# Kernel tuning notes

Hardware: AMD Instinct MI355X
Metric: run time of the kernel (lower is better)

Reference implementation:

```python
import jax, jax.numpy as jnp
import numpy as np

G, N, D, H, R, O = 16384, 32, 128, 256, 32, 64  # graphs, nodes/graph, input_dim, hidden_dim, rank_dim, output_dim


def _xavier_uniform(key, shape):
    fan_in, fan_out = shape[0], shape[1]
    a = jnp.sqrt(6.0 / (fan_in + fan_out))
    return jax.random.uniform(key, shape, minval=-a, maxval=a, dtype=jnp.float32)


def setup_inputs() -> dict:
    key = jax.random.key(0)
    k_h, k_W, k_V, k_Wl, k_bl = jax.random.split(key, 5)
    h = jax.random.normal(k_h, (G, N, D), dtype=jnp.float32)
    W = _xavier_uniform(k_W, (D, R))          # graph_cp_pooling.W
    V = _xavier_uniform(k_V, (H, R))          # graph_cp_pooling.V
    Wl = _xavier_uniform(k_Wl, (O, H))        # linears_prediction[0].weight
    bl = jnp.zeros((O,), dtype=jnp.float32)   # linears_prediction[0].bias
    return {"h": h, "W": W, "V": V, "Wl": Wl, "bl": bl}


def reference(h, W, V, Wl, bl):
    # graph_cp_pooling (init=True), vectorized over graphs:
    #   feat_g = h_g @ W          -> [G, N, R]
    #   pooled = prod over nodes  -> [G, R]
    #   readout = pooled @ V.T    -> [G, H]
    feat = jnp.einsum('gnd,dr->gnr', h, W)
    pooled = jnp.prod(feat, axis=1)
    readout = pooled @ V.T
    # linears_prediction[0]; dropout is identity in eval mode
    score = readout @ Wl.T + bl
    return score
```

## Files before the change

### kernel.cpp

```cpp
#include <hip/hip_runtime.h>
#include <math.h>

#define NG  16384
#define NN  32
#define DD  128
#define RR  32
#define OO  64
#define HHH 256

__global__ void precompute_M_kernel(const float* __restrict__ Wl,
                                    const float* __restrict__ V,
                                    float* __restrict__ M) {
    int t = blockIdx.x * blockDim.x + threadIdx.x;
    int o = t >> 5;
    int r = t & 31;
    float s = 0.f;
#pragma unroll 8
    for (int hh = 0; hh < HHH; ++hh)
        s = fmaf(Wl[o * HHH + hh], V[hh * RR + r], s);
    M[o * RR + r] = s;
}

__device__ __forceinline__ void fma4(float4& a, float s, const float4& w) {
    a.x = fmaf(s, w.x, a.x);
    a.y = fmaf(s, w.y, a.y);
    a.z = fmaf(s, w.z, a.z);
    a.w = fmaf(s, w.w, a.w);
}

typedef const float __attribute__((address_space(1))) gfloat;
typedef float       __attribute__((address_space(3))) lfloat;

__global__ __launch_bounds__(256, 2)
void gin_main_kernel(const float* __restrict__ hsrc,
                     const float* __restrict__ W,
                     const float* __restrict__ M,
                     const float* __restrict__ bl,
                     float* __restrict__ out) {
    __shared__ float sW[DD * RR];
    __shared__ float sH[4][NN * 32];

    const int tid  = threadIdx.x;
    const int lane = tid & 63;
    const int wv   = tid >> 6;

    {
        const float4* Wv  = (const float4*)W;
        float4*       sWv = (float4*)sW;
#pragma unroll
        for (int k = 0; k < 4; ++k) sWv[tid + k * 256] = Wv[tid + k * 256];
    }
    __syncthreads();

    const int rg = lane & 7;
    const int ng = lane >> 3;
    const int r0 = rg * 4;
    float* sHw = sH[wv];
    const int rowl = lane >> 3;
    const int tq   = lane & 7;
    const float* pWb = sW + r0;

    const int wave_global = blockIdx.x * 4 + wv;
    const float blv = bl[lane];

#pragma unroll 1
    for (int gi = 0; gi < 4; ++gi) {
        const int g = wave_global * 4 + gi;
        const float* hg = hsrc + (size_t)g * (NN * DD);

        float4 acc0 = make_float4(0.f, 0.f, 0.f, 0.f);
        float4 acc1 = acc0, acc2 = acc0, acc3 = acc0;

#pragma unroll
        for (int c = 0; c < 4; ++c) {
#pragma unroll
            for (int l = 0; l < 4; ++l) {
                const int row = l * 8 + rowl;
                const int sq  = (tq + row) & 7;
                const float* gp = hg + row * DD + c * 32 + sq * 4;
                __builtin_amdgcn_global_load_lds((gfloat*)gp,
                                                 (lfloat*)(sHw + l * 256),
                                                 16, 0, 0);
            }
            asm volatile("s_waitcnt vmcnt(0)" ::: "memory");

            const float* ph = sHw + ng * 32;
#pragma unroll
            for (int q = 0; q < 8; ++q) {
                const int d = c * 32 + q * 4;
                const int hq = ((q - ng) & 7) * 4;
                float4 w0 = *(const float4*)(pWb + (d + 0) * RR);
                float4 w1 = *(const float4*)(pWb + (d + 1) * RR);
                float4 w2 = *(const float4*)(pWb + (d + 2) * RR);
                float4 w3 = *(const float4*)(pWb + (d + 3) * RR);
                float4 h0 = *(const float4*)(ph + 0 * 256 + hq);
                float4 h1 = *(const float4*)(ph + 1 * 256 + hq);
                float4 h2 = *(const float4*)(ph + 2 * 256 + hq);
                float4 h3 = *(const float4*)(ph + 3 * 256 + hq);
                fma4(acc0, h0.x, w0); fma4(acc0, h0.y, w1); fma4(acc0, h0.z, w2); fma4(acc0, h0.w, w3);
                fma4(acc1, h1.x, w0); fma4(acc1, h1.y, w1); fma4(acc1, h1.z, w2); fma4(acc1, h1.w, w3);
                fma4(acc2, h2.x, w0); fma4(acc2, h2.y, w1); fma4(acc2, h2.z, w2); fma4(acc2, h2.w, w3);
                fma4(acc3, h3.x, w0); fma4(acc3, h3.y, w1); fma4(acc3, h3.z, w2); fma4(acc3, h3.w, w3);
            }
        }

        float4 p;
        p.x = acc0.x * acc1.x * acc2.x * acc3.x;
        p.y = acc0.y * acc1.y * acc2.y * acc3.y;
        p.z = acc0.z * acc1.z * acc2.z * acc3.z;
        p.w = acc0.w * acc1.w * acc2.w * acc3.w;
#pragma unroll
        for (int m = 8; m <= 32; m <<= 1) {
            p.x *= __shfl_xor(p.x, m);
            p.y *= __shfl_xor(p.y, m);
            p.z *= __shfl_xor(p.z, m);
            p.w *= __shfl_xor(p.w, m);
        }

        const float4* Mv = (const float4*)(M + lane * RR);
        float s = blv;
#pragma unroll
        for (int rq = 0; rq < 8; ++rq) {
            float4 pq;
            pq.x = __shfl(p.x, rq);
            pq.y = __shfl(p.y, rq);
            pq.z = __shfl(p.z, rq);
            pq.w = __shfl(p.w, rq);
            float4 m4 = Mv[rq];
            s = fmaf(pq.x, m4.x, s);
            s = fmaf(pq.y, m4.y, s);
            s = fmaf(pq.z, m4.z, s);
            s = fmaf(pq.w, m4.w, s);
        }
        out[(size_t)g * OO + lane] = s;
    }
}

extern "C" void kernel_launch(void* const* d_in, const int* in_sizes, int n_in,
                              void* d_out, int out_size, void* d_ws, size_t ws_size,
                              hipStream_t stream) {
    const float* h  = (const float*)d_in[0];
    const float* W  = (const float*)d_in[1];
    const float* V  = (const float*)d_in[2];
    const float* Wl = (const float*)d_in[3];
    const float* bl = (const float*)d_in[4];
    float* out = (float*)d_out;
    float* M   = (float*)d_ws;

    precompute_M_kernel<<<8, 256, 0, stream>>>(Wl, V, M);
    gin_main_kernel<<<1024, 256, 0, stream>>>(h, W, M, bl, out);
}
```

Before: 388.2 us.

## Remap threads to one node per lane with double-buffered LDS chunk loads

Each lane now computes all 32 rank outputs for one node of one of two graphs. W is read directly from global memory with wave-uniform addresses, so the shared-memory copy of W goes away. The h chunks are double-buffered in LDS so the next chunk's async loads overlap the current chunk's FMAs. The product over nodes becomes a 5-step xor-shuffle reduction over 32 accumulators, and M is held in registers for the final projection. This raises register pressure a lot (32 accumulators plus 64 floats of M) and relies on scalar or cached loads of W to hide the global read latency.

```diff
diff --git a/kernel.cpp b/kernel.cpp
--- a/kernel.cpp
+++ b/kernel.cpp
@@ -21,118 +21,114 @@
     M[o * RR + r] = s;
 }
 
-__device__ __forceinline__ void fma4(float4& a, float s, const float4& w) {
-    a.x = fmaf(s, w.x, a.x);
-    a.y = fmaf(s, w.y, a.y);
-    a.z = fmaf(s, w.z, a.z);
-    a.w = fmaf(s, w.w, a.w);
-}
-
 typedef const float __attribute__((address_space(1))) gfloat;
 typedef float       __attribute__((address_space(3))) lfloat;
 
-__global__ __launch_bounds__(256, 2)
+__global__ __launch_bounds__(128, 2)
 void gin_main_kernel(const float* __restrict__ hsrc,
                      const float* __restrict__ W,
                      const float* __restrict__ M,
                      const float* __restrict__ bl,
                      float* __restrict__ out) {
-    __shared__ float sW[DD * RR];
-    __shared__ float sH[4][NN * 32];
+    __shared__ float sH[2][2][2048];
 
     const int tid  = threadIdx.x;
     const int lane = tid & 63;
     const int wv   = tid >> 6;
+    const int n    = lane & 31;
+    const int gh   = lane >> 5;
+    const int rowL = lane >> 3;
+    const int s8   = lane & 7;
+    const int qoff = ((s8 - rowL) & 7) * 4;
 
+    const int waveId = blockIdx.x * 2 + wv;
+
+    float4 Mr0[8], Mr1[8];
     {
-        const float4* Wv  = (const float4*)W;
-        float4*       sWv = (float4*)sW;
+        const float4* M0 = (const float4*)(M + n * RR);
+        const float4* M1 = (const float4*)(M + (n + 32) * RR);
 #pragma unroll
-        for (int k = 0; k < 4; ++k) sWv[tid + k * 256] = Wv[tid + k * 256];
+        for (int i = 0; i < 8; ++i) { Mr0[i] = M0[i]; Mr1[i] = M1[i]; }
     }
-    __syncthreads();
+    const float bl0 = bl[n], bl1 = bl[n + 32];
 
-    const int rg = lane & 7;
-    const int ng = lane >> 3;
-    const int r0 = rg * 4;
-    float* sHw = sH[wv];
-    const int rowl = lane >> 3;
-    const int tq   = lane & 7;
-    const float* pWb = sW + r0;
-
-    const int wave_global = blockIdx.x * 4 + wv;
-    const float blv = bl[lane];
+    auto issue_chunk = [&](const float* hg0, const float* hg1, int c, int slot) {
+        float* dstb = &sH[wv][slot][0];
+        const int goff = c * 32 + qoff;
+#pragma unroll
+        for (int j = 0; j < 4; ++j) {
+            const float* gp = hg0 + (j * 8 + rowL) * DD + goff;
+            __builtin_amdgcn_global_load_lds((gfloat*)gp, (lfloat*)(dstb + j * 256), 16, 0, 0);
+        }
+#pragma unroll
+        for (int j = 0; j < 4; ++j) {
+            const float* gp = hg1 + (j * 8 + rowL) * DD + goff;
+            __builtin_amdgcn_global_load_lds((gfloat*)gp, (lfloat*)(dstb + 1024 + j * 256), 16, 0, 0);
+        }
+    };
 
 #pragma unroll 1
-    for (int gi = 0; gi < 4; ++gi) {
-        const int g = wave_global * 4 + gi;
-        const float* hg = hsrc + (size_t)g * (NN * DD);
+    for (int pi = 0; pi < 2; ++pi) {
+        const int g0 = waveId * 4 + pi * 2;
+        const float* hg0 = hsrc + (size_t)g0 * (NN * DD);
+        const float* hg1 = hg0 + NN * DD;
 
-        float4 acc0 = make_float4(0.f, 0.f, 0.f, 0.f);
-        float4 acc1 = acc0, acc2 = acc0, acc3 = acc0;
+        float acc[32];
+#pragma unroll
+        for (int r = 0; r < 32; ++r) acc[r] = 0.f;
+
+        issue_chunk(hg0, hg1, 0, 0);
+        issue_chunk(hg0, hg1, 1, 1);
 
 #pragma unroll
         for (int c = 0; c < 4; ++c) {
+            if (c < 3) asm volatile("s_waitcnt vmcnt(8)" ::: "memory");
+            else       asm volatile("s_waitcnt vmcnt(0)" ::: "memory");
+
+            const float* ph = &sH[wv][c & 1][gh * 1024 + n * 32];
+            const float* Wc = W + c * 32 * RR;
+#pragma unroll 2
+            for (int dq = 0; dq < 8; ++dq) {
+                float4 hq = *(const float4*)(ph + ((dq + n) & 7) * 4);
+                const float4* wr = (const float4*)(Wc + dq * 4 * RR);
 #pragma unroll
-            for (int l = 0; l < 4; ++l) {
-                const int row = l * 8 + rowl;
-                const int sq  = (tq + row) & 7;
-                const float* gp = hg + row * DD + c * 32 + sq * 4;
-                __builtin_amdgcn_global_load_lds((gfloat*)gp,
-                                                 (lfloat*)(sHw + l * 256),
-                                                 16, 0, 0);
+                for (int r4 = 0; r4 < 8; ++r4) {
+                    float4 w0 = wr[r4];
+                    float4 w1 = wr[8 + r4];
+                    float4 w2 = wr[16 + r4];
+                    float4 w3 = wr[24 + r4];
+                    acc[r4*4+0] = fmaf(hq.w, w3.x, fmaf(hq.z, w2.x, fmaf(hq.y, w1.x, fmaf(hq.x, w0.x, acc[r4*4+0]))));
+                    acc[r4*4+1] = fmaf(hq.w, w3.y, fmaf(hq.z, w2.y, fmaf(hq.y, w1.y, fmaf(hq.x, w0.y, acc[r4*4+1]))));
+                    acc[r4*4+2] = fmaf(hq.w, w3.z, fmaf(hq.z, w2.z, fmaf(hq.y, w1.z, fmaf(hq.x, w0.z, acc[r4*4+2]))));
+                    acc[r4*4+3] = fmaf(hq.w, w3.w, fmaf(hq.z, w2.w, fmaf(hq.y, w1.w, fmaf(hq.x, w0.w, acc[r4*4+3]))));
+                }
             }
-            asm volatile("s_waitcnt vmcnt(0)" ::: "memory");
-
-            const float* ph = sHw + ng * 32;
-#pragma unroll
-            for (int q = 0; q < 8; ++q) {
-                const int d = c * 32 + q * 4;
-                const int hq = ((q - ng) & 7) * 4;
-                float4 w0 = *(const float4*)(pWb + (d + 0) * RR);
-                float4 w1 = *(const float4*)(pWb + (d + 1) * RR);
-                float4 w2 = *(const float4*)(pWb + (d + 2) * RR);
-                float4 w3 = *(const float4*)(pWb + (d + 3) * RR);
-                float4 h0 = *(const float4*)(ph + 0 * 256 + hq);
-                float4 h1 = *(const float4*)(ph + 1 * 256 + hq);
-                float4 h2 = *(const float4*)(ph + 2 * 256 + hq);
-                float4 h3 = *(const float4*)(ph + 3 * 256 + hq);
-                fma4(acc0, h0.x, w0); fma4(acc0, h0.y, w1); fma4(acc0, h0.z, w2); fma4(acc0, h0.w, w3);
-                fma4(acc1, h1.x, w0); fma4(acc1, h1.y, w1); fma4(acc1, h1.z, w2); fma4(acc1, h1.w, w3);
-                fma4(acc2, h2.x, w0); fma4(acc2, h2.y, w1); fma4(acc2, h2.z, w2); fma4(acc2, h2.w, w3);
-                fma4(acc3, h3.x, w0); fma4(acc3, h3.y, w1); fma4(acc3, h3.z, w2); fma4(acc3, h3.w, w3);
-            }
+            if (c < 2) issue_chunk(hg0, hg1, c + 2, c & 1);
         }
 
-        float4 p;
-        p.x = acc0.x * acc1.x * acc2.x * acc3.x;
-        p.y = acc0.y * acc1.y * acc2.y * acc3.y;
-        p.z = acc0.z * acc1.z * acc2.z * acc3.z;
-        p.w = acc0.w * acc1.w * acc2.w * acc3.w;
 #pragma unroll
-        for (int m = 8; m <= 32; m <<= 1) {
-            p.x *= __shfl_xor(p.x, m);
-            p.y *= __shfl_xor(p.y, m);
-            p.z *= __shfl_xor(p.z, m);
-            p.w *= __shfl_xor(p.w, m);
+        for (int m = 1; m <= 16; m <<= 1) {
+#pragma unroll
+            for (int r = 0; r < 32; ++r)
+                acc[r] *= __shfl_xor(acc[r], m);
         }
 
-        const float4* Mv = (const float4*)(M + lane * RR);
-        float s = blv;
+        float s0 = bl0, s1 = bl1;
 #pragma unroll
-        for (int rq = 0; rq < 8; ++rq) {
-            float4 pq;
-            pq.x = __shfl(p.x, rq);
-            pq.y = __shfl(p.y, rq);
-            pq.z = __shfl(p.z, rq);
-            pq.w = __shfl(p.w, rq);
-            float4 m4 = Mv[rq];
-            s = fmaf(pq.x, m4.x, s);
-            s = fmaf(pq.y, m4.y, s);
-            s = fmaf(pq.z, m4.z, s);
-            s = fmaf(pq.w, m4.w, s);
+        for (int i = 0; i < 8; ++i) {
+            float4 m0 = Mr0[i], m1 = Mr1[i];
+            s0 = fmaf(acc[i*4+0], m0.x, s0);
+            s0 = fmaf(acc[i*4+1], m0.y, s0);
+            s0 = fmaf(acc[i*4+2], m0.z, s0);
+            s0 = fmaf(acc[i*4+3], m0.w, s0);
+            s1 = fmaf(acc[i*4+0], m1.x, s1);
+            s1 = fmaf(acc[i*4+1], m1.y, s1);
+            s1 = fmaf(acc[i*4+2], m1.z, s1);
+            s1 = fmaf(acc[i*4+3], m1.w, s1);
         }
-        out[(size_t)g * OO + lane] = s;
+        float* og = out + (size_t)(g0 + gh) * OO;
+        og[n]      = s0;
+        og[n + 32] = s1;
     }
 }
 
@@ -148,5 +144,5 @@
     float* M   = (float*)d_ws;
 
     precompute_M_kernel<<<8, 256, 0, stream>>>(Wl, V, M);
-    gin_main_kernel<<<1024, 256, 0, stream>>>(h, W, M, bl, out);
+    gin_main_kernel<<<2048, 128, 0, stream>>>(h, W, M, bl, out);
 }
```

Result: slower. 419.3 us (+8.0%).

## Load node features directly into registers with prefetch and transpose projection matrix

Applied to the files above, without the earlier changes.

The global-to-LDS staging of node features, with a full vmcnt wait per chunk, is replaced by direct float4 global loads into registers. A two-stage software prefetch overlaps the next loads with the current FMAs. The fused Wl·V matrix is stored transposed so each lane reads a coalesced column, and the pooled product is broadcast through a small LDS buffer instead of lane shuffles. Lanes with the same node group now load identical addresses, and each load instruction touches eight separate rows, so coalescing is weaker and depends on cache reuse.

```diff
diff --git a/kernel.cpp b/kernel.cpp
--- a/kernel.cpp
+++ b/kernel.cpp
@@ -8,9 +8,9 @@
 #define OO  64
 #define HHH 256
 
-__global__ void precompute_M_kernel(const float* __restrict__ Wl,
-                                    const float* __restrict__ V,
-                                    float* __restrict__ M) {
+__global__ void precompute_MT_kernel(const float* __restrict__ Wl,
+                                     const float* __restrict__ V,
+                                     float* __restrict__ MT) {
     int t = blockIdx.x * blockDim.x + threadIdx.x;
     int o = t >> 5;
     int r = t & 31;
@@ -18,7 +18,7 @@
 #pragma unroll 8
     for (int hh = 0; hh < HHH; ++hh)
         s = fmaf(Wl[o * HHH + hh], V[hh * RR + r], s);
-    M[o * RR + r] = s;
+    MT[r * OO + o] = s;
 }
 
 __device__ __forceinline__ void fma4(float4& a, float s, const float4& w) {
@@ -28,21 +28,21 @@
     a.w = fmaf(s, w.w, a.w);
 }
 
-typedef const float __attribute__((address_space(1))) gfloat;
-typedef float       __attribute__((address_space(3))) lfloat;
-
 __global__ __launch_bounds__(256, 2)
 void gin_main_kernel(const float* __restrict__ hsrc,
                      const float* __restrict__ W,
-                     const float* __restrict__ M,
+                     const float* __restrict__ MT,
                      const float* __restrict__ bl,
                      float* __restrict__ out) {
     __shared__ float sW[DD * RR];
-    __shared__ float sH[4][NN * 32];
+    __shared__ float sP[4][32];
 
     const int tid  = threadIdx.x;
     const int lane = tid & 63;
     const int wv   = tid >> 6;
+    const int rg   = lane & 7;
+    const int ng   = lane >> 3;
+    const int r0   = rg * 4;
 
     {
         const float4* Wv  = (const float4*)W;
@@ -50,65 +50,66 @@
 #pragma unroll
         for (int k = 0; k < 4; ++k) sWv[tid + k * 256] = Wv[tid + k * 256];
     }
+    const float blv = bl[lane];
     __syncthreads();
 
-    const int rg = lane & 7;
-    const int ng = lane >> 3;
-    const int r0 = rg * 4;
-    float* sHw = sH[wv];
-    const int rowl = lane >> 3;
-    const int tq   = lane & 7;
+    const int gbase = (blockIdx.x * 4 + wv) * 4;
     const float* pWb = sW + r0;
-
-    const int wave_global = blockIdx.x * 4 + wv;
-    const float blv = bl[lane];
 
 #pragma unroll 1
     for (int gi = 0; gi < 4; ++gi) {
-        const int g = wave_global * 4 + gi;
-        const float* hg = hsrc + (size_t)g * (NN * DD);
+        const int g = gbase + gi;
+        const float* ph = hsrc + (size_t)g * (NN * DD) + ng * DD;
 
-        float4 acc0 = make_float4(0.f, 0.f, 0.f, 0.f);
-        float4 acc1 = acc0, acc2 = acc0, acc3 = acc0;
+        float4 a0 = make_float4(0.f, 0.f, 0.f, 0.f);
+        float4 a1 = a0, a2 = a0, a3 = a0;
 
-#pragma unroll
-        for (int c = 0; c < 4; ++c) {
-#pragma unroll
-            for (int l = 0; l < 4; ++l) {
-                const int row = l * 8 + rowl;
-                const int sq  = (tq + row) & 7;
-                const float* gp = hg + row * DD + c * 32 + sq * 4;
-                __builtin_amdgcn_global_load_lds((gfloat*)gp,
-                                                 (lfloat*)(sHw + l * 256),
-                                                 16, 0, 0);
+        float4 c0 = *(const float4*)(ph + 0 * 1024 + 0);
+        float4 c1 = *(const float4*)(ph + 1 * 1024 + 0);
+        float4 c2 = *(const float4*)(ph + 2 * 1024 + 0);
+        float4 c3 = *(const float4*)(ph + 3 * 1024 + 0);
+
+#pragma unroll 1
+        for (int dq = 0; dq < 32; dq += 2) {
+            float4 n0 = *(const float4*)(ph + 0 * 1024 + (dq + 1) * 4);
+            float4 n1 = *(const float4*)(ph + 1 * 1024 + (dq + 1) * 4);
+            float4 n2 = *(const float4*)(ph + 2 * 1024 + (dq + 1) * 4);
+            float4 n3 = *(const float4*)(ph + 3 * 1024 + (dq + 1) * 4);
+            {
+                const float* pW = pWb + dq * 4 * RR;
+                float4 w0 = *(const float4*)(pW + 0 * RR);
+                float4 w1 = *(const float4*)(pW + 1 * RR);
+                float4 w2 = *(const float4*)(pW + 2 * RR);
+                float4 w3 = *(const float4*)(pW + 3 * RR);
+                fma4(a0, c0.x, w0); fma4(a0, c0.y, w1); fma4(a0, c0.z, w2); fma4(a0, c0.w, w3);
+                fma4(a1, c1.x, w0); fma4(a1, c1.y, w1); fma4(a1, c1.z, w2); fma4(a1, c1.w, w3);
+                fma4(a2, c2.x, w0); fma4(a2, c2.y, w1); fma4(a2, c2.z, w2); fma4(a2, c2.w, w3);
+                fma4(a3, c3.x, w0); fma4(a3, c3.y, w1); fma4(a3, c3.z, w2); fma4(a3, c3.w, w3);
             }
-            asm volatile("s_waitcnt vmcnt(0)" ::: "memory");
-
-            const float* ph = sHw + ng * 32;
-#pragma unroll
-            for (int q = 0; q < 8; ++q) {
-                const int d = c * 32 + q * 4;
-                const int hq = ((q - ng) & 7) * 4;
-                float4 w0 = *(const float4*)(pWb + (d + 0) * RR);
-                float4 w1 = *(const float4*)(pWb + (d + 1) * RR);
-                float4 w2 = *(const float4*)(pWb + (d + 2) * RR);
-                float4 w3 = *(const float4*)(pWb + (d + 3) * RR);
-                float4 h0 = *(const float4*)(ph + 0 * 256 + hq);
-                float4 h1 = *(const float4*)(ph + 1 * 256 + hq);
-                float4 h2 = *(const float4*)(ph + 2 * 256 + hq);
-                float4 h3 = *(const float4*)(ph + 3 * 256 + hq);
-                fma4(acc0, h0.x, w0); fma4(acc0, h0.y, w1); fma4(acc0, h0.z, w2); fma4(acc0, h0.w, w3);
-                fma4(acc1, h1.x, w0); fma4(acc1, h1.y, w1); fma4(acc1, h1.z, w2); fma4(acc1, h1.w, w3);
-                fma4(acc2, h2.x, w0); fma4(acc2, h2.y, w1); fma4(acc2, h2.z, w2); fma4(acc2, h2.w, w3);
-                fma4(acc3, h3.x, w0); fma4(acc3, h3.y, w1); fma4(acc3, h3.z, w2); fma4(acc3, h3.w, w3);
+            if (dq < 30) {
+                c0 = *(const float4*)(ph + 0 * 1024 + (dq + 2) * 4);
+                c1 = *(const float4*)(ph + 1 * 1024 + (dq + 2) * 4);
+                c2 = *(const float4*)(ph + 2 * 1024 + (dq + 2) * 4);
+                c3 = *(const float4*)(ph + 3 * 1024 + (dq + 2) * 4);
+            }
+            {
+                const float* pW = pWb + (dq + 1) * 4 * RR;
+                float4 w0 = *(const float4*)(pW + 0 * RR);
+                float4 w1 = *(const float4*)(pW + 1 * RR);
+                float4 w2 = *(const float4*)(pW + 2 * RR);
+                float4 w3 = *(const float4*)(pW + 3 * RR);
+                fma4(a0, n0.x, w0); fma4(a0, n0.y, w1); fma4(a0, n0.z, w2); fma4(a0, n0.w, w3);
+                fma4(a1, n1.x, w0); fma4(a1, n1.y, w1); fma4(a1, n1.z, w2); fma4(a1, n1.w, w3);
+                fma4(a2, n2.x, w0); fma4(a2, n2.y, w1); fma4(a2, n2.z, w2); fma4(a2, n2.w, w3);
+                fma4(a3, n3.x, w0); fma4(a3, n3.y, w1); fma4(a3, n3.z, w2); fma4(a3, n3.w, w3);
             }
         }
 
         float4 p;
-        p.x = acc0.x * acc1.x * acc2.x * acc3.x;
-        p.y = acc0.y * acc1.y * acc2.y * acc3.y;
-        p.z = acc0.z * acc1.z * acc2.z * acc3.z;
-        p.w = acc0.w * acc1.w * acc2.w * acc3.w;
+        p.x = a0.x * a1.x * a2.x * a3.x;
+        p.y = a0.y * a1.y * a2.y * a3.y;
+        p.z = a0.z * a1.z * a2.z * a3.z;
+        p.w = a0.w * a1.w * a2.w * a3.w;
 #pragma unroll
         for (int m = 8; m <= 32; m <<= 1) {
             p.x *= __shfl_xor(p.x, m);
@@ -116,21 +117,16 @@
             p.z *= __shfl_xor(p.z, m);
             p.w *= __shfl_xor(p.w, m);
         }
+        if (ng == 0) *(float4*)(&sP[wv][r0]) = p;
 
-        const float4* Mv = (const float4*)(M + lane * RR);
         float s = blv;
 #pragma unroll
         for (int rq = 0; rq < 8; ++rq) {
-            float4 pq;
-            pq.x = __shfl(p.x, rq);
-            pq.y = __shfl(p.y, rq);
-            pq.z = __shfl(p.z, rq);
-            pq.w = __shfl(p.w, rq);
-            float4 m4 = Mv[rq];
-            s = fmaf(pq.x, m4.x, s);
-            s = fmaf(pq.y, m4.y, s);
-            s = fmaf(pq.z, m4.z, s);
-            s = fmaf(pq.w, m4.w, s);
+            float4 pq = *(const float4*)(&sP[wv][rq * 4]);
+            s = fmaf(pq.x, MT[(rq * 4 + 0) * OO + lane], s);
+            s = fmaf(pq.y, MT[(rq * 4 + 1) * OO + lane], s);
+            s = fmaf(pq.z, MT[(rq * 4 + 2) * OO + lane], s);
+            s = fmaf(pq.w, MT[(rq * 4 + 3) * OO + lane], s);
         }
         out[(size_t)g * OO + lane] = s;
     }
@@ -145,8 +141,8 @@
     const float* Wl = (const float*)d_in[3];
     const float* bl = (const float*)d_in[4];
     float* out = (float*)d_out;
-    float* M   = (float*)d_ws;
+    float* MT  = (float*)d_ws;
 
-    precompute_M_kernel<<<8, 256, 0, stream>>>(Wl, V, M);
-    gin_main_kernel<<<1024, 256, 0, stream>>>(h, W, M, bl, out);
+    precompute_MT_kernel<<<8, 256, 0, stream>>>(Wl, V, MT);
+    gin_main_kernel<<<1024, 256, 0, stream>>>(h, W, MT, bl, out);
 }
```

New measurement: 432.2 us. +11.3%, slower.
